# Kernel optimization log

Hardware: AMD Instinct MI355X
Metric: run time of the kernel (lower is better)

The kernel has to match this reference:

```python
import jax, jax.numpy as jnp
import numpy as np

EPS = 1e-3  # BatchNorm1d eps


def _fc_relu(x, W, b):
    return jax.nn.relu(x @ W + b)


def _fc_bn_relu(x, W, b, gamma, beta):
    # Linear -> BatchNorm1d (training mode: batch stats, biased var) -> ReLU
    h = x @ W + b
    m = jnp.mean(h, axis=0)
    v = jnp.var(h, axis=0)  # biased, matches torch BN normalization
    return jax.nn.relu((h - m) * jax.lax.rsqrt(v + EPS) * gamma + beta)


def _mmnet(img, tag, lat, lon, Wi, bi, gi, bti, Wt, bt, gt, btt, Wl, bl, gl, btl,
           W1, b1, W2, b2, W3, b3, W4, b4, W5, b5, W6, b6, W7, b7):
    img = _fc_bn_relu(img, Wi, bi, gi, bti)          # [B,300]
    tag = _fc_bn_relu(tag, Wt, bt, gt, btt)          # [B,300]
    loc = jnp.concatenate([lat, lon], axis=1)        # [B,2]
    loc = _fc_bn_relu(loc, Wl, bl, gl, btl)          # [B,10]
    x = jnp.concatenate([loc, img, tag], axis=1)     # [B,610]
    x = _fc_relu(x, W1, b1)                          # [B,2048]
    x = _fc_relu(x, W2, b2)                          # [B,2048]
    x = _fc_relu(x, W3, b3)                          # [B,1024]
    x = _fc_relu(x, W4, b4)                          # [B,1024]
    x = _fc_relu(x, W5, b5)                          # [B,512]
    x = _fc_relu(x, W6, b6)                          # [B,512]
    return x @ W7 + b7                               # [B,1]


def setup_inputs() -> dict:
    key = jax.random.key(0)
    ks = iter(jax.random.split(key, 64))
    B = 16384
    inp = {}
    inp['img_p'] = jax.random.normal(next(ks), (B, 300), jnp.float32)
    inp['tag_p'] = jax.random.normal(next(ks), (B, 300), jnp.float32)
    inp['lat_p'] = jax.random.uniform(next(ks), (B, 1), jnp.float32)
    inp['lon_p'] = jax.random.uniform(next(ks), (B, 1), jnp.float32)
    inp['img_n'] = jax.random.normal(next(ks), (B, 300), jnp.float32)
    inp['tag_n'] = jax.random.normal(next(ks), (B, 300), jnp.float32)
    inp['lat_n'] = jax.random.uniform(next(ks), (B, 1), jnp.float32)
    inp['lon_n'] = jax.random.uniform(next(ks), (B, 1), jnp.float32)
    inp['margin'] = 1

    def lin(din, dout):
        # matches l.weight.data.normal_(0, 0.01), bias zero; stored [din,dout]
        return (jax.random.normal(next(ks), (din, dout), jnp.float32) * 0.01,
                jnp.zeros((dout,), jnp.float32))

    inp['Wi'], inp['bi'] = lin(300, 300)
    inp['gi'], inp['bti'] = jnp.ones((300,), jnp.float32), jnp.zeros((300,), jnp.float32)
    inp['Wt'], inp['bt'] = lin(300, 300)
    inp['gt'], inp['btt'] = jnp.ones((300,), jnp.float32), jnp.zeros((300,), jnp.float32)
    inp['Wl'], inp['bl'] = lin(2, 10)
    inp['gl'], inp['btl'] = jnp.ones((10,), jnp.float32), jnp.zeros((10,), jnp.float32)
    inp['W1'], inp['b1'] = lin(610, 2048)
    inp['W2'], inp['b2'] = lin(2048, 2048)
    inp['W3'], inp['b3'] = lin(2048, 1024)
    inp['W4'], inp['b4'] = lin(1024, 1024)
    inp['W5'], inp['b5'] = lin(1024, 512)
    inp['W6'], inp['b6'] = lin(512, 512)
    inp['W7'], inp['b7'] = lin(512, 1)
    return inp


def reference(img_p, tag_p, lat_p, lon_p, img_n, tag_n, lat_n, lon_n,
              Wi, bi, gi, bti, Wt, bt, gt, btt, Wl, bl, gl, btl,
              W1, b1, W2, b2, W3, b3, W4, b4, W5, b5, W6, b6, W7, b7, margin):
    params = (Wi, bi, gi, bti, Wt, bt, gt, btt, Wl, bl, gl, btl,
              W1, b1, W2, b2, W3, b3, W4, b4, W5, b5, W6, b6, W7, b7)
    score_p = _mmnet(img_p, tag_p, lat_p, lon_p, *params)  # [B,1]
    score_n = _mmnet(img_n, tag_n, lat_n, lon_n, *params)  # [B,1]
    # vectorized replacement of the per-element python loop
    correct = jnp.sum((score_p - score_n)[:, 0] > margin).astype(jnp.int32)
    return score_p, score_n, correct
```

## Files before the change

### kernel.cpp

```cpp
#include <hip/hip_runtime.h>
#include <hip/hip_fp16.h>

typedef _Float16 half8 __attribute__((ext_vector_type(8)));
typedef float f32x16 __attribute__((ext_vector_type(16)));

#define B_ROWS 16384
#define M_ALL  32768

__device__ __forceinline__ void glds16(void* lds, const void* g) {
  __builtin_amdgcn_global_load_lds(
      (const __attribute__((address_space(1))) unsigned int*)g,
      (__attribute__((address_space(3))) unsigned int*)lds, 16, 0, 0);
}

template<int EPI>
__global__ __launch_bounds__(256, 2)
void gemm128(const _Float16* __restrict__ A, const _Float16* __restrict__ Bt,
             const float* __restrict__ bias, _Float16* __restrict__ Cout,
             int M, int N, int K) {
  __shared__ _Float16 As[128 * 64];
  __shared__ _Float16 Bs[128 * 64];
  const int tid = threadIdx.x;
  const int w = tid >> 6, l = tid & 63;
  const int bm = blockIdx.y << 7, bn = blockIdx.x << 7;
  const int wm = (w >> 1) << 6, wn = (w & 1) << 6;
  const int l31 = l & 31, g5 = l >> 5, l7 = l & 7, l3 = l >> 3;

  f32x16 acc[2][2];
#pragma unroll
  for (int i = 0; i < 2; ++i)
#pragma unroll
    for (int j = 0; j < 2; ++j)
#pragma unroll
      for (int r = 0; r < 16; ++r) acc[i][j][r] = 0.f;

  const int schunk = (l7 ^ l3) * 8;
  const int srow = w * 32 + l3;

  for (int kt = 0; kt < K; kt += 64) {
#pragma unroll
    for (int c = 0; c < 4; ++c)
      glds16(&As[w * 2048 + c * 512],
             A + (size_t)(bm + srow + c * 8) * K + kt + schunk);
#pragma unroll
    for (int c = 0; c < 4; ++c)
      glds16(&Bs[w * 2048 + c * 512],
             Bt + (size_t)(bn + srow + c * 8) * K + kt + schunk);
    __syncthreads();
#pragma unroll
    for (int ks = 0; ks < 4; ++ks) {
      const int p0 = (((ks * 2 + g5) ^ l7)) * 8;
      half8 af[2], bf[2];
#pragma unroll
      for (int i = 0; i < 2; ++i)
        af[i] = *(const half8*)&As[(wm + i * 32 + l31) * 64 + p0];
#pragma unroll
      for (int i = 0; i < 2; ++i)
        bf[i] = *(const half8*)&Bs[(wn + i * 32 + l31) * 64 + p0];
#pragma unroll
      for (int i = 0; i < 2; ++i)
#pragma unroll
        for (int j = 0; j < 2; ++j)
          acc[i][j] = __builtin_amdgcn_mfma_f32_32x32x16_f16(af[i], bf[j], acc[i][j], 0, 0, 0);
    }
    __syncthreads();
  }

#pragma unroll
  for (int i = 0; i < 2; ++i)
#pragma unroll
    for (int j = 0; j < 2; ++j) {
      const int col = bn + wn + j * 32 + l31;
      float bv = 0.f;
      if (EPI == 1) bv = bias[col];
#pragma unroll
      for (int r = 0; r < 16; ++r) {
        const int row = bm + wm + i * 32 + (r & 3) + 8 * (r >> 2) + 4 * g5;
        const float v = acc[i][j][r] + bv;
        Cout[(size_t)row * N + col] = (_Float16)(EPI == 1 ? fmaxf(v, 0.f) : v);
      }
    }
}

__global__ __launch_bounds__(512, 1)
void gemm256(const _Float16* __restrict__ A, const _Float16* __restrict__ Bt,
             const float* __restrict__ bias, _Float16* __restrict__ Cout,
             int M, int N, int K) {
  __shared__ _Float16 smem[4 * 256 * 64];
  const int tid = threadIdx.x;
  const int w = tid >> 6, l = tid & 63;
  const int bm = blockIdx.y << 8, bn = blockIdx.x << 8;
  const int wm = w >> 2, wn = w & 3;
  const int l31 = l & 31, g5 = l >> 5, l7 = l & 7, l3 = l >> 3;

  f32x16 acc[4][2];
#pragma unroll
  for (int i = 0; i < 4; ++i)
#pragma unroll
    for (int j = 0; j < 2; ++j)
#pragma unroll
      for (int r = 0; r < 16; ++r) acc[i][j][r] = 0.f;

  const int schunk = (l7 ^ l3) * 8;
  const _Float16* aSrc = A + (size_t)(bm + w * 32 + l3) * K + schunk;
  const _Float16* bSrc = Bt + (size_t)(bn + w * 32 + l3) * K + schunk;
  const int NT = K >> 6;

  auto stage = [&](int buf, int t) {
    _Float16* as = smem + buf * 16384;
    _Float16* bs = smem + 32768 + buf * 16384;
    const size_t ko = (size_t)t * 64;
#pragma unroll
    for (int c = 0; c < 4; ++c)
      glds16(as + (w * 32 + c * 8) * 64, aSrc + (size_t)c * 8 * K + ko);
#pragma unroll
    for (int c = 0; c < 4; ++c)
      glds16(bs + (w * 32 + c * 8) * 64, bSrc + (size_t)c * 8 * K + ko);
  };

  stage(0, 0);
  stage(1, 1);
  asm volatile("s_waitcnt vmcnt(8)" ::: "memory");
  __builtin_amdgcn_s_barrier();

  half8 bf[2][4];
  for (int t = 0; t < NT; ++t) {
    const _Float16* as = smem + (t & 1) * 16384;
    const _Float16* bs = smem + 32768 + (t & 1) * 16384;
#pragma unroll
    for (int p = 0; p < 4; ++p) {
      half8 af[4];
#pragma unroll
      for (int ks = 0; ks < 4; ++ks)
        af[ks] = *(const half8*)(as + (wm * 128 + p * 32 + l31) * 64
                                    + ((ks * 2 + g5) ^ l7) * 8);
      if (p == 0) {
#pragma unroll
        for (int j = 0; j < 2; ++j)
#pragma unroll
          for (int ks = 0; ks < 4; ++ks)
            bf[j][ks] = *(const half8*)(bs + (wn * 64 + j * 32 + l31) * 64
                                           + ((ks * 2 + g5) ^ l7) * 8);
      }
      __builtin_amdgcn_s_barrier();
      asm volatile("s_waitcnt lgkmcnt(0)" ::: "memory");
      __builtin_amdgcn_sched_barrier(0);
      __builtin_amdgcn_s_setprio(1);
#pragma unroll
      for (int ks = 0; ks < 4; ++ks)
#pragma unroll
        for (int j = 0; j < 2; ++j)
          acc[p][j] = __builtin_amdgcn_mfma_f32_32x32x16_f16(
              af[ks], bf[j][ks], acc[p][j], 0, 0, 0);
      __builtin_amdgcn_s_setprio(0);
      if (p < 3) __builtin_amdgcn_s_barrier();
    }
    asm volatile("s_waitcnt vmcnt(0)" ::: "memory");
    __builtin_amdgcn_s_barrier();
    if (t + 2 < NT) stage(t & 1, t + 2);
  }

#pragma unroll
  for (int mi = 0; mi < 4; ++mi)
#pragma unroll
    for (int nj = 0; nj < 2; ++nj) {
      const int col = bn + wn * 64 + nj * 32 + l31;
      const float bv = bias[col];
#pragma unroll
      for (int r = 0; r < 16; ++r) {
        const int row = bm + wm * 128 + mi * 32 + (r & 3) + 8 * (r >> 2) + 4 * g5;
        Cout[(size_t)row * N + col] = (_Float16)fmaxf(acc[mi][nj][r] + bv, 0.f);
      }
    }
}

__global__ void tpose_pad(const float* __restrict__ src, _Float16* __restrict__ dst,
                          int Ks, int Ns, int Kd, int Nd) {
  __shared__ float t[32][33];
  const int k0 = blockIdx.x * 32, n0 = blockIdx.y * 32;
  const int tx = threadIdx.x & 31, ty = threadIdx.x >> 5;
#pragma unroll
  for (int i = ty; i < 32; i += 8) {
    const int k = k0 + i, n = n0 + tx;
    t[i][tx] = (k < Ks && n < Ns) ? src[(size_t)k * Ns + n] : 0.f;
  }
  __syncthreads();
#pragma unroll
  for (int i = ty; i < 32; i += 8)
    dst[(size_t)(n0 + i) * Kd + (k0 + tx)] = (_Float16)t[tx][i];
}

__global__ void cvt_in_k(const float* __restrict__ xp, const float* __restrict__ xn,
                         _Float16* __restrict__ X, int C, int Cp) {
  const size_t total = (size_t)M_ALL * Cp;
  const size_t stride = (size_t)gridDim.x * blockDim.x;
  for (size_t idx = (size_t)blockIdx.x * blockDim.x + threadIdx.x; idx < total; idx += stride) {
    const int r = (int)(idx / Cp);
    const int c = (int)(idx - (size_t)r * Cp);
    float v = 0.f;
    if (c < C) v = (r < B_ROWS) ? xp[(size_t)r * C + c] : xn[(size_t)(r - B_ROWS) * C + c];
    X[idx] = (_Float16)v;
  }
}

__global__ void stats_k(const _Float16* __restrict__ h, float* __restrict__ sums, int ldh, int C) {
  const int half = blockIdx.y;
  const int nr = B_ROWS / gridDim.x;
  const int r0 = half * B_ROWS + blockIdx.x * nr;
  for (int c = threadIdx.x; c < C; c += blockDim.x) {
    float s = 0.f, q = 0.f;
    for (int r = 0; r < nr; ++r) {
      const float v = (float)h[(size_t)(r0 + r) * ldh + c];
      s += v; q += v * v;
    }
    atomicAdd(&sums[(half * 2 + 0) * 384 + c], s);
    atomicAdd(&sums[(half * 2 + 1) * 384 + c], q);
  }
}

__global__ void bn_apply_k(const _Float16* __restrict__ h, const float* __restrict__ sums,
                           const float* __restrict__ gamma, const float* __restrict__ beta,
                           _Float16* __restrict__ X1, int coff) {
  const size_t total = (size_t)M_ALL * 300;
  const size_t stride = (size_t)gridDim.x * blockDim.x;
  for (size_t idx = (size_t)blockIdx.x * blockDim.x + threadIdx.x; idx < total; idx += stride) {
    const int r = (int)(idx / 300);
    const int c = (int)(idx - (size_t)r * 300);
    const int hf = r >> 14;
    const float mean = sums[(hf * 2 + 0) * 384 + c] * (1.f / 16384.f);
    const float ms   = sums[(hf * 2 + 1) * 384 + c] * (1.f / 16384.f);
    const float inv = rsqrtf(ms - mean * mean + 1e-3f) * gamma[c];
    const float y = ((float)h[(size_t)r * 384 + c] - mean) * inv + beta[c];
    X1[(size_t)r * 640 + coff + c] = (_Float16)fmaxf(y, 0.f);
  }
}

__global__ void loc_k(const float* __restrict__ lat_p, const float* __restrict__ lon_p,
                      const float* __restrict__ lat_n, const float* __restrict__ lon_n,
                      const float* __restrict__ Wl, const float* __restrict__ gl,
                      const float* __restrict__ btl, _Float16* __restrict__ X1) {
  const int j = blockIdx.x, half = blockIdx.y;
  const float* lat = half ? lat_n : lat_p;
  const float* lon = half ? lon_n : lon_p;
  const float w0 = Wl[j], w1 = Wl[10 + j];
  const int t = threadIdx.x;
  float s = 0.f, q = 0.f;
  for (int r = t; r < B_ROWS; r += 256) {
    const float v = lat[r] * w0 + lon[r] * w1;
    s += v; q += v * v;
  }
  __shared__ float rs[256], rq[256];
  rs[t] = s; rq[t] = q;
  __syncthreads();
  for (int o = 128; o; o >>= 1) {
    if (t < o) { rs[t] += rs[t + o]; rq[t] += rq[t + o]; }
    __syncthreads();
  }
  const float mean = rs[0] * (1.f / 16384.f);
  const float var = rq[0] * (1.f / 16384.f) - mean * mean;
  const float inv = rsqrtf(var + 1e-3f) * gl[j];
  const float bb = btl[j];
  for (int r = t; r < B_ROWS; r += 256) {
    const float v = lat[r] * w0 + lon[r] * w1;
    const float y = (v - mean) * inv + bb;
    X1[(size_t)(half * B_ROWS + r) * 640 + j] = (_Float16)fmaxf(y, 0.f);
  }
}

__global__ void scores_k(const _Float16* __restrict__ Y, const float* __restrict__ w7,
                         const float* __restrict__ b7, float* __restrict__ out) {
  const int row = blockIdx.x * 4 + (threadIdx.x >> 6);
  const int l = threadIdx.x & 63;
  const half8 v = *(const half8*)(Y + (size_t)row * 512 + l * 8);
  float s = 0.f;
#pragma unroll
  for (int j = 0; j < 8; ++j) s += (float)v[j] * w7[l * 8 + j];
#pragma unroll
  for (int o = 32; o; o >>= 1) s += __shfl_down(s, o);
  if (l == 0) out[row] = s + b7[0];
}

__global__ void correct_k(const float* __restrict__ sc, const int* __restrict__ mg,
                          float* __restrict__ dst) {
  __shared__ int red[256];
  const int t = threadIdx.x;
  const float m = (float)(*mg);
  int c = 0;
  for (int i = t; i < B_ROWS; i += 256)
    c += (sc[i] - sc[B_ROWS + i]) > m ? 1 : 0;
  red[t] = c;
  __syncthreads();
  for (int o = 128; o; o >>= 1) {
    if (t < o) red[t] += red[t + o];
    __syncthreads();
  }
  if (t == 0) dst[0] = (float)red[0];
}

extern "C" void kernel_launch(void* const* d_in, const int* in_sizes, int n_in,
                              void* d_out, int out_size, void* d_ws, size_t ws_size,
                              hipStream_t stream) {
  const float* img_p = (const float*)d_in[0];
  const float* tag_p = (const float*)d_in[1];
  const float* lat_p = (const float*)d_in[2];
  const float* lon_p = (const float*)d_in[3];
  const float* img_n = (const float*)d_in[4];
  const float* tag_n = (const float*)d_in[5];
  const float* lat_n = (const float*)d_in[6];
  const float* lon_n = (const float*)d_in[7];
  const int*   margin = (const int*)d_in[8];
  const float* Wi = (const float*)d_in[9];
  const float* gi = (const float*)d_in[11];
  const float* bti = (const float*)d_in[12];
  const float* Wt = (const float*)d_in[13];
  const float* gt = (const float*)d_in[15];
  const float* btt = (const float*)d_in[16];
  const float* Wl = (const float*)d_in[17];
  const float* gl = (const float*)d_in[19];
  const float* btl = (const float*)d_in[20];
  const float* W1 = (const float*)d_in[21]; const float* b1 = (const float*)d_in[22];
  const float* W2 = (const float*)d_in[23]; const float* b2 = (const float*)d_in[24];
  const float* W3 = (const float*)d_in[25]; const float* b3 = (const float*)d_in[26];
  const float* W4 = (const float*)d_in[27]; const float* b4 = (const float*)d_in[28];
  const float* W5 = (const float*)d_in[29]; const float* b5 = (const float*)d_in[30];
  const float* W6 = (const float*)d_in[31]; const float* b6 = (const float*)d_in[32];
  const float* W7 = (const float*)d_in[33]; const float* b7 = (const float*)d_in[34];
  float* out = (float*)d_out;

  char* ws = (char*)d_ws;
  size_t off = 0;
  auto alloc = [&](size_t bytes) -> void* {
    void* p = ws + off;
    off += (bytes + 255) & ~(size_t)255;
    return p;
  };
  _Float16* WiT = (_Float16*)alloc((size_t)384 * 320 * 2);
  _Float16* WtT = (_Float16*)alloc((size_t)384 * 320 * 2);
  _Float16* W1T = (_Float16*)alloc((size_t)2048 * 640 * 2);
  _Float16* W2T = (_Float16*)alloc((size_t)2048 * 2048 * 2);
  _Float16* W3T = (_Float16*)alloc((size_t)1024 * 2048 * 2);
  _Float16* W4T = (_Float16*)alloc((size_t)1024 * 1024 * 2);
  _Float16* W5T = (_Float16*)alloc((size_t)512 * 1024 * 2);
  _Float16* W6T = (_Float16*)alloc((size_t)512 * 512 * 2);
  float* sbuf = (float*)alloc((size_t)2 * 4 * 384 * 4);
  _Float16* X1 = (_Float16*)alloc((size_t)M_ALL * 640 * 2);

  const size_t persist = off;
  const size_t avail = ws_size > persist ? ws_size - persist : 0;
  int CR = 4096;
  if (avail >= (size_t)2 * 32768 * 2048 * 2) CR = 32768;
  else if (avail >= (size_t)2 * 16384 * 2048 * 2) CR = 16384;
  else if (avail >= (size_t)2 * 8192 * 2048 * 2) CR = 8192;
  _Float16* Ya = (_Float16*)(ws + persist);
  _Float16* Yb = Ya + (size_t)CR * 2048;
  _Float16* Ximg = Ya;
  _Float16* hbuf = (_Float16*)((char*)Ya + (size_t)M_ALL * 320 * 2);

  (void)hipMemsetAsync(X1, 0, (size_t)M_ALL * 640 * 2, stream);
  (void)hipMemsetAsync(sbuf, 0, (size_t)2 * 4 * 384 * 4, stream);

  tpose_pad<<<dim3(10, 12), 256, 0, stream>>>(Wi, WiT, 300, 300, 320, 384);
  tpose_pad<<<dim3(10, 12), 256, 0, stream>>>(Wt, WtT, 300, 300, 320, 384);
  tpose_pad<<<dim3(20, 64), 256, 0, stream>>>(W1, W1T, 610, 2048, 640, 2048);
  tpose_pad<<<dim3(64, 64), 256, 0, stream>>>(W2, W2T, 2048, 2048, 2048, 2048);
  tpose_pad<<<dim3(64, 32), 256, 0, stream>>>(W3, W3T, 2048, 1024, 2048, 1024);
  tpose_pad<<<dim3(32, 32), 256, 0, stream>>>(W4, W4T, 1024, 1024, 1024, 1024);
  tpose_pad<<<dim3(32, 16), 256, 0, stream>>>(W5, W5T, 1024, 512, 1024, 512);
  tpose_pad<<<dim3(16, 16), 256, 0, stream>>>(W6, W6T, 512, 512, 512, 512);

  cvt_in_k<<<2048, 256, 0, stream>>>(img_p, img_n, Ximg, 300, 320);
  gemm128<2><<<dim3(3, 256), 256, 0, stream>>>(Ximg, WiT, nullptr, hbuf, M_ALL, 384, 320);
  stats_k<<<dim3(128, 2), 256, 0, stream>>>(hbuf, sbuf, 384, 300);
  bn_apply_k<<<2048, 256, 0, stream>>>(hbuf, sbuf, gi, bti, X1, 10);
  cvt_in_k<<<2048, 256, 0, stream>>>(tag_p, tag_n, Ximg, 300, 320);
  gemm128<2><<<dim3(3, 256), 256, 0, stream>>>(Ximg, WtT, nullptr, hbuf, M_ALL, 384, 320);
  stats_k<<<dim3(128, 2), 256, 0, stream>>>(hbuf, sbuf + 4 * 384, 384, 300);
  bn_apply_k<<<2048, 256, 0, stream>>>(hbuf, sbuf + 4 * 384, gt, btt, X1, 310);
  loc_k<<<dim3(10, 2), 256, 0, stream>>>(lat_p, lon_p, lat_n, lon_n, Wl, gl, btl, X1);

  for (int c0 = 0; c0 < M_ALL; c0 += CR) {
    const int rb = CR / 128, rb2 = CR / 256;
    const _Float16* Xc = X1 + (size_t)c0 * 640;
    gemm256<<<dim3(8, rb2), 512, 0, stream>>>(Xc, W1T, b1, Ya, CR, 2048, 640);
    gemm256<<<dim3(8, rb2), 512, 0, stream>>>(Ya, W2T, b2, Yb, CR, 2048, 2048);
    gemm256<<<dim3(4, rb2), 512, 0, stream>>>(Yb, W3T, b3, Ya, CR, 1024, 2048);
    gemm256<<<dim3(4, rb2), 512, 0, stream>>>(Ya, W4T, b4, Yb, CR, 1024, 1024);
    gemm128<1><<<dim3(4, rb), 256, 0, stream>>>(Yb, W5T, b5, Ya, CR, 512, 1024);
    gemm128<1><<<dim3(4, rb), 256, 0, stream>>>(Ya, W6T, b6, Yb, CR, 512, 512);
    scores_k<<<CR / 4, 256, 0, stream>>>(Yb, W7, b7, out + c0);
  }

  correct_k<<<1, 256, 0, stream>>>(out, margin, out + 32768);
}
```

Measured before the change: 1.027 ms.

## Switch gemm256 to 16x16x32 MFMA with new LDS swizzle and XCD-aware block remap

Rewrites the 256x256 GEMM inner loop to use 16x16x32 f16 MFMA tiles (8x4 accumulators per wave) in place of 32x32x16. It loads all A/B fragments for a K-tile up front, removes the intra-tile barriers, and changes the LDS XOR swizzle to match the new fragment access pattern. It also remaps workgroup IDs so consecutive blocks spread across the 8 XCDs, aiming for better L2 locality. The risks are higher register pressure from holding 24 half8 fragments plus 32 accumulators, and possible LDS bank conflicts if the new swizzle is not conflict-free.

```diff
diff --git a/kernel.cpp b/kernel.cpp
--- a/kernel.cpp
+++ b/kernel.cpp
@@ -3,6 +3,7 @@
 
 typedef _Float16 half8 __attribute__((ext_vector_type(8)));
 typedef float f32x16 __attribute__((ext_vector_type(16)));
+typedef float f32x4 __attribute__((ext_vector_type(4)));
 
 #define B_ROWS 16384
 #define M_ALL  32768
@@ -89,19 +90,25 @@
   __shared__ _Float16 smem[4 * 256 * 64];
   const int tid = threadIdx.x;
   const int w = tid >> 6, l = tid & 63;
-  const int bm = blockIdx.y << 8, bn = blockIdx.x << 8;
+  const int nwg = gridDim.x * gridDim.y;
+  const int orig = blockIdx.y * gridDim.x + blockIdx.x;
+  const int wgid = (orig & 7) * (nwg >> 3) + (orig >> 3);
+  const int bx = wgid % gridDim.x, by = wgid / gridDim.x;
+  const int bm = by << 8, bn = bx << 8;
   const int wm = w >> 2, wn = w & 3;
-  const int l31 = l & 31, g5 = l >> 5, l7 = l & 7, l3 = l >> 3;
-
-  f32x16 acc[4][2];
-#pragma unroll
-  for (int i = 0; i < 4; ++i)
-#pragma unroll
-    for (int j = 0; j < 2; ++j)
-#pragma unroll
-      for (int r = 0; r < 16; ++r) acc[i][j][r] = 0.f;
-
-  const int schunk = (l7 ^ l3) * 8;
+  const int l15 = l & 15, kh = (l >> 4) & 3;
+  const int rx = ((l >> 2) & 1) << 1;
+  const int l3 = l >> 3;
+
+  f32x4 acc[8][4];
+#pragma unroll
+  for (int i = 0; i < 8; ++i)
+#pragma unroll
+    for (int j = 0; j < 4; ++j)
+#pragma unroll
+      for (int r = 0; r < 4; ++r) acc[i][j][r] = 0.f;
+
+  const int schunk = ((l & 7) ^ (((l >> 5) & 1) << 1)) * 8;
   const _Float16* aSrc = A + (size_t)(bm + w * 32 + l3) * K + schunk;
   const _Float16* bSrc = Bt + (size_t)(bn + w * 32 + l3) * K + schunk;
   const int NT = K >> 6;
@@ -123,55 +130,48 @@
   asm volatile("s_waitcnt vmcnt(8)" ::: "memory");
   __builtin_amdgcn_s_barrier();
 
-  half8 bf[2][4];
   for (int t = 0; t < NT; ++t) {
     const _Float16* as = smem + (t & 1) * 16384;
     const _Float16* bs = smem + 32768 + (t & 1) * 16384;
-#pragma unroll
-    for (int p = 0; p < 4; ++p) {
-      half8 af[4];
-#pragma unroll
-      for (int ks = 0; ks < 4; ++ks)
-        af[ks] = *(const half8*)(as + (wm * 128 + p * 32 + l31) * 64
-                                    + ((ks * 2 + g5) ^ l7) * 8);
-      if (p == 0) {
-#pragma unroll
-        for (int j = 0; j < 2; ++j)
-#pragma unroll
-          for (int ks = 0; ks < 4; ++ks)
-            bf[j][ks] = *(const half8*)(bs + (wn * 64 + j * 32 + l31) * 64
-                                           + ((ks * 2 + g5) ^ l7) * 8);
-      }
-      __builtin_amdgcn_s_barrier();
-      asm volatile("s_waitcnt lgkmcnt(0)" ::: "memory");
-      __builtin_amdgcn_sched_barrier(0);
-      __builtin_amdgcn_s_setprio(1);
-#pragma unroll
-      for (int ks = 0; ks < 4; ++ks)
-#pragma unroll
-        for (int j = 0; j < 2; ++j)
-          acc[p][j] = __builtin_amdgcn_mfma_f32_32x32x16_f16(
-              af[ks], bf[j][ks], acc[p][j], 0, 0, 0);
-      __builtin_amdgcn_s_setprio(0);
-      if (p < 3) __builtin_amdgcn_s_barrier();
-    }
+    half8 af[2][8], bf[2][4];
+#pragma unroll
+    for (int t2 = 0; t2 < 2; ++t2) {
+      const int pc = ((t2 * 4 + kh) ^ rx) * 8;
+#pragma unroll
+      for (int mi = 0; mi < 8; ++mi)
+        af[t2][mi] = *(const half8*)(as + (wm * 128 + mi * 16 + l15) * 64 + pc);
+#pragma unroll
+      for (int nj = 0; nj < 4; ++nj)
+        bf[t2][nj] = *(const half8*)(bs + (wn * 64 + nj * 16 + l15) * 64 + pc);
+    }
+    __builtin_amdgcn_s_setprio(1);
+#pragma unroll
+    for (int t2 = 0; t2 < 2; ++t2)
+#pragma unroll
+      for (int mi = 0; mi < 8; ++mi)
+#pragma unroll
+        for (int nj = 0; nj < 4; ++nj)
+          acc[mi][nj] = __builtin_amdgcn_mfma_f32_16x16x32_f16(
+              af[t2][mi], bf[t2][nj], acc[mi][nj], 0, 0, 0);
+    __builtin_amdgcn_s_setprio(0);
     asm volatile("s_waitcnt vmcnt(0)" ::: "memory");
     __builtin_amdgcn_s_barrier();
     if (t + 2 < NT) stage(t & 1, t + 2);
   }
 
 #pragma unroll
-  for (int mi = 0; mi < 4; ++mi)
-#pragma unroll
-    for (int nj = 0; nj < 2; ++nj) {
-      const int col = bn + wn * 64 + nj * 32 + l31;
-      const float bv = bias[col];
-#pragma unroll
-      for (int r = 0; r < 16; ++r) {
-        const int row = bm + wm * 128 + mi * 32 + (r & 3) + 8 * (r >> 2) + 4 * g5;
+  for (int nj = 0; nj < 4; ++nj) {
+    const int col = bn + wn * 64 + nj * 16 + l15;
+    const float bv = bias[col];
+#pragma unroll
+    for (int mi = 0; mi < 8; ++mi) {
+#pragma unroll
+      for (int r = 0; r < 4; ++r) {
+        const int row = bm + wm * 128 + mi * 16 + ((l >> 4) << 2) + r;
         Cout[(size_t)row * N + col] = (_Float16)fmaxf(acc[mi][nj][r] + bv, 0.f);
       }
     }
+  }
 }
 
 __global__ void tpose_pad(const float* __restrict__ src, _Float16* __restrict__ dst,
```

Measured after the change: 963.3 us. 1.07x faster.
